# Optimization experiments

Hardware: AMD Instinct MI355X
Metric: run time of the kernel (lower is better)

## Reference

```python
import jax, jax.numpy as jnp
import numpy as np
import math

ITERATIONS = 2
STRIDE = 1
ALPHA = 0.0
MEAN_DATA = 1.0
FINAL_LAMBDA = 0.01  # final_beta
EPS = 1e-7
MIN_VAR_ADD = 0.0005


def setup_inputs() -> dict:
    key = jax.random.key(0)
    k1, k2 = jax.random.split(key)
    b, h, w, k, i, o, a = 2, 12, 12, 3, 32, 32, 4
    votes = jax.random.normal(k1, (b, h, w, k, k, i, o, a, a), dtype=jnp.float32)
    acts = jax.random.uniform(k2, (b, h, w, k, k, i, 1, 1, 1), dtype=jnp.float32)
    beta_a = jnp.full((1, 1, 1, 1, 1, 1, o, 1, 1), 0.5, dtype=jnp.float32)
    beta_u = jnp.full((1, 1, 1, 1, 1, 1, o, 1, 1), 0.5, dtype=jnp.float32)
    return {"votes": votes, "acts": acts, "beta_a": beta_a, "beta_u": beta_u}


def reference(votes, acts, beta_a, beta_u):
    b, h, w, k = votes.shape[0], votes.shape[1], votes.shape[2], votes.shape[3]
    i, o, a = votes.shape[5], votes.shape[6], votes.shape[7]
    s = STRIDE
    Hr = h * s + k - s  # reconstructed height
    Wr = w * s + k - s
    # target spatial coords for each (h,y) / (w,x) of the kernel window
    Y = jnp.arange(h)[:, None] * s + jnp.arange(k)[None, :]  # (h,k)
    X = jnp.arange(w)[:, None] * s + jnp.arange(k)[None, :]  # (w,k)
    lin = (Y[:, None, :, None] * Wr + X[None, :, None, :]).reshape(-1)  # (h*w*k*k,)

    # R_ij init: softmax over zeros along out-capsule axis -> uniform 1/o
    R = jnp.full((b, h, w, k, k, i, o, 1, 1), 1.0 / o, dtype=votes.dtype)
    out_poses = jnp.zeros((b, h, w, 1, 1, 1, o, a, a), dtype=votes.dtype)

    def m_step(R, out_poses, it):
        Ra = R * acts                                   # (b,h,w,k,k,i,o,1,1)
        sumR = jnp.sum(Ra, axis=(3, 4, 5), keepdims=True)
        mu = jnp.sum(Ra * votes, axis=(3, 4, 5), keepdims=True) / (sumR + EPS)
        mu = (1.0 - ALPHA) * mu + ALPHA * out_poses     # (b,h,w,1,1,1,o,a,a)
        sig = jnp.sum(Ra * jnp.square(votes - mu), axis=(3, 4, 5), keepdims=True) / (sumR + EPS) + MIN_VAR_ADD
        cost = (beta_u - 0.5 * jnp.log(sig + EPS)) * sumR / MEAN_DATA
        inv_temp = FINAL_LAMBDA * (1.0 - 0.95 ** (it + 1))
        a_j = jax.nn.sigmoid(inv_temp * (beta_a - jnp.sum(cost, axis=(-1, -2), keepdims=True)))
        return mu, sig, a_j

    def e_step(mu, sig, a_j):
        log_p = -jnp.sum(jnp.log(2.0 * math.pi * sig) + jnp.square(votes - mu) / (2.0 * sig),
                         axis=(-1, -2), keepdims=True)        # (b,h,w,k,k,i,o,1,1)
        lognum = jnp.log(a_j) + log_p
        ap = jnp.exp(lognum - jnp.max(lognum))                # global-max shift as in original
        # scatter-add (fold / col2im) onto the reconstructed grid, then sum over o
        ap6 = ap.reshape(b, h, w, k, k, i, o)
        ap_t = ap6.transpose(1, 2, 3, 4, 0, 5, 6).reshape(h * w * k * k, b, i, o)
        dense = jax.ops.segment_sum(ap_t, lin, num_segments=Hr * Wr)  # (Hr*Wr,b,i,o)
        dense = dense.sum(-1).reshape(Hr, Wr, b, i)
        # extract_patches: gather the window sums back to (b,h,w,k,k,i)
        denom = dense[Y[:, None, :, None], X[None, :, None, :]]  # (h,w,k,k,b,i)
        denom = jnp.transpose(denom, (4, 0, 1, 2, 3, 5))[..., None, None, None]
        return ap / (denom + EPS)

    for it in range(ITERATIONS - 1):
        mu, sig, a_j = m_step(R, out_poses, it)
        out_poses = mu
        R = e_step(mu, sig, a_j)
    mu, sig, a_j = m_step(R, out_poses, ITERATIONS)

    poses = jnp.squeeze(mu, axis=(3, 4, 5))     # (b,h,w,o,a,a)
    acts_out = jnp.squeeze(a_j, axis=(3, 4, 5))  # (b,h,w,o,1,1)
    return poses, acts_out
```

## Files before the change

### kernel.cpp

```cpp
#include <hip/hip_runtime.h>
#include <math.h>

#define NB 2
#define NH 12
#define NW 12
#define NK 3
#define NI 32
#define NO 32
#define NBHW (NB*NH*NW)
#define NC (NK*NK*NI)
#define VPB (NC*NO*16)
#define HR 14
#define WR 14
#define EPSF 1e-7f
#define MINVAR 5e-4f
#define TEMP0 0.0005f
#define TEMPF 0.00142625f

#define CH 4
#define CPC (NC/CH)
#define NBLK (NBHW*CH)
#define ITERS (CPC/2)

#define DENSE_N (NB*HR*WR*NI)
#define DENSE_OFF 0
#define S1_OFF    (DENSE_OFF + DENSE_N)
#define S2_OFF    (S1_OFF + NBLK*512)
#define SR_OFF    (S2_OFF + NBLK*512)
#define MU_OFF    (SR_OFF + NBLK)
#define W_OFF     (MU_OFF + NBHW*512)
#define L_OFF     (W_OFF + NBHW*512)
#define BM_OFF    (L_OFF + NBHW*32)
#define M_OFF     (BM_OFF + NBLK)
#define LOG_OFF   (M_OFF + 4)
#define DSR_OFF   (LOG_OFF + NBHW*NC*NO)

__global__ __launch_bounds__(256) void kA(const float* __restrict__ votes,
        const float* __restrict__ acts, float* __restrict__ ws) {
    __shared__ float s_acts[CPC];
    __shared__ float4 r1[128], r2[128];
    __shared__ float sR1;
    const int bid = blockIdx.x;
    const int bhw = bid >> 2;
    const int cbase = (bid & 3) * CPC;
    const int t = threadIdx.x;
    {
        const int idx = bid*256 + t;
        if (idx < DENSE_N) ws[DENSE_OFF + idx] = 0.f;
    }
    if (t < CPC) s_acts[t] = acts[bhw*NC + cbase + t] * (1.0f/NO);
    __syncthreads();
    const int child_sub = t >> 7;
    const int rem = t & 127;
    const float4* vb4 = (const float4*)votes + (size_t)bhw*(VPB/4);
    float s1[4] = {0,0,0,0}, s2[4] = {0,0,0,0};
    float sumR = 0.f;
    #pragma unroll 6
    for (int it = 0; it < ITERS; ++it) {
        const int c_loc = it*2 + child_sub;
        float4 v = vb4[(size_t)(cbase + c_loc)*128 + rem];
        float ra = s_acts[c_loc];
        s1[0] += ra*v.x; s2[0] = fmaf(ra*v.x, v.x, s2[0]);
        s1[1] += ra*v.y; s2[1] = fmaf(ra*v.y, v.y, s2[1]);
        s1[2] += ra*v.z; s2[2] = fmaf(ra*v.z, v.z, s2[2]);
        s1[3] += ra*v.w; s2[3] = fmaf(ra*v.w, v.w, s2[3]);
        sumR += ra;
    }
    if (child_sub) {
        r1[rem] = make_float4(s1[0], s1[1], s1[2], s1[3]);
        r2[rem] = make_float4(s2[0], s2[1], s2[2], s2[3]);
        if (rem == 0) sR1 = sumR;
    }
    __syncthreads();
    if (!child_sub) {
        float4 o1 = r1[rem], o2 = r2[rem];
        ((float4*)(ws + S1_OFF))[bid*128 + rem] =
            make_float4(s1[0]+o1.x, s1[1]+o1.y, s1[2]+o1.z, s1[3]+o1.w);
        ((float4*)(ws + S2_OFF))[bid*128 + rem] =
            make_float4(s2[0]+o2.x, s2[1]+o2.y, s2[2]+o2.z, s2[3]+o2.w);
        if (rem == 0) ws[SR_OFF + bid] = sumR + sR1;
    }
}

__global__ __launch_bounds__(256) void kB0(const float* __restrict__ beta_a,
        const float* __restrict__ beta_u, float* __restrict__ ws) {
    const int bhw = blockIdx.x;
    const int t = threadIdx.x;
    float sumR = 0.f;
    #pragma unroll
    for (int s = 0; s < CH; ++s) sumR += ws[SR_OFF + bhw*CH + s];
    #pragma unroll
    for (int half = 0; half < 2; ++half) {
        const int idx = t + half*256;
        float s1 = 0.f, s2 = 0.f;
        #pragma unroll
        for (int s = 0; s < CH; ++s) {
            s1 += ws[S1_OFF + (size_t)(bhw*CH + s)*512 + idx];
            s2 += ws[S2_OFF + (size_t)(bhw*CH + s)*512 + idx];
        }
        const int o = idx >> 4, a = idx & 15;
        float mu  = s1 / (sumR + EPSF);
        float sig = (s2 - mu*(2.f*s1 - mu*sumR)) / (sumR + EPSF) + MINVAR;
        ws[MU_OFF + bhw*512 + a*32 + o] = mu;
        ws[W_OFF  + bhw*512 + a*32 + o] = 0.5f / sig;
        float cost = (beta_u[o] - 0.5f*logf(sig + EPSF)) * sumR;
        float ps   = logf(6.2831853071795864f * sig);
        #pragma unroll
        for (int d = 1; d < 16; d <<= 1) {
            cost += __shfl_xor(cost, d);
            ps   += __shfl_xor(ps, d);
        }
        if (a == 0) {
            float aj = 1.0f/(1.0f + expf(-TEMP0*(beta_a[o] - cost)));
            ws[L_OFF + bhw*32 + o] = logf(aj) - ps;
        }
    }
}

__global__ __launch_bounds__(256) void kB(const float* __restrict__ votes,
        float* __restrict__ ws) {
    __shared__ float s_mu[512], s_w[512], s_L[32], smax[4];
    const int bid = blockIdx.x;
    const int bhw = bid >> 2;
    const int cbase = (bid & 3) * CPC;
    const int t = threadIdx.x;
    s_mu[t]     = ws[MU_OFF + bhw*512 + t];
    s_mu[t+256] = ws[MU_OFF + bhw*512 + t + 256];
    s_w[t]      = ws[W_OFF + bhw*512 + t];
    s_w[t+256]  = ws[W_OFF + bhw*512 + t + 256];
    if (t < 32) s_L[t] = ws[L_OFF + bhw*32 + t];
    __syncthreads();
    const int child_sub = t >> 7;
    const int rem = t & 127;
    const int o = rem >> 2;
    const int quad = rem & 3;
    float mur[4], wr[4];
    #pragma unroll
    for (int j = 0; j < 4; ++j) {
        mur[j] = s_mu[(quad*4 + j)*32 + o];
        wr[j]  = s_w [(quad*4 + j)*32 + o];
    }
    const float L = s_L[o];
    const float4* vb4 = (const float4*)votes + (size_t)bhw*(VPB/4);
    float* lp = ws + LOG_OFF + (size_t)bhw*(NC*NO);
    float tmax = -3.0e38f;
    #pragma unroll 6
    for (int it = 0; it < ITERS; ++it) {
        const int c = cbase + it*2 + child_sub;
        float4 v = vb4[(size_t)c*128 + rem];
        float d0 = v.x - mur[0];
        float acc = d0*d0*wr[0];
        float d1 = v.y - mur[1]; acc = fmaf(d1*d1, wr[1], acc);
        float d2 = v.z - mur[2]; acc = fmaf(d2*d2, wr[2], acc);
        float d3 = v.w - mur[3]; acc = fmaf(d3*d3, wr[3], acc);
        acc += __shfl_xor(acc, 1);
        acc += __shfl_xor(acc, 2);
        float ln = L - acc;
        if (quad == 0) lp[c*32 + o] = ln;
        tmax = fmaxf(tmax, ln);
    }
    #pragma unroll
    for (int d = 1; d < 64; d <<= 1) tmax = fmaxf(tmax, __shfl_xor(tmax, d));
    if ((t & 63) == 0) smax[t >> 6] = tmax;
    __syncthreads();
    if (t == 0)
        ws[BM_OFF + bid] = fmaxf(fmaxf(smax[0], smax[1]), fmaxf(smax[2], smax[3]));
}

__global__ __launch_bounds__(256) void kC0(float* __restrict__ ws) {
    __shared__ float smax[4];
    const int t = threadIdx.x;
    float m = -3.0e38f;
    for (int i = t; i < NBLK; i += 256) m = fmaxf(m, ws[BM_OFF + i]);
    #pragma unroll
    for (int d = 1; d < 64; d <<= 1) m = fmaxf(m, __shfl_xor(m, d));
    if ((t & 63) == 0) smax[t >> 6] = m;
    __syncthreads();
    if (t == 0)
        ws[M_OFF] = fmaxf(fmaxf(smax[0], smax[1]), fmaxf(smax[2], smax[3]));
}

__global__ __launch_bounds__(256) void kC(float* __restrict__ ws) {
    const int bid = blockIdx.x;
    const int bhw = bid >> 2;
    const int cbase = (bid & 3) * CPC;
    const int t = threadIdx.x;
    const float M = ws[M_OFF];
    const int b = bhw / (NH*NW);
    const int rem = bhw % (NH*NW);
    const int y = rem / NW, x = rem % NW;
    const float* lp = ws + LOG_OFF + (size_t)bhw*(NC*NO);
    float* dense = ws + DENSE_OFF;
    const int o = t & 31;
    for (int it = 0; it < CPC/8; ++it) {
        const int c = cbase + it*8 + (t >> 5);
        float s = expf(lp[c*32 + o] - M);
        #pragma unroll
        for (int d = 1; d < 32; d <<= 1) s += __shfl_xor(s, d);
        if (o == 0) {
            const int i = c & 31, kk = c >> 5;
            const int ky = kk / 3, kx = kk % 3;
            atomicAdd(&dense[((b*HR + y+ky)*WR + (x+kx))*NI + i], s);
        }
    }
}

__global__ __launch_bounds__(256) void kD(const float* __restrict__ votes,
        const float* __restrict__ acts, float* __restrict__ ws) {
    __shared__ float s_rd[CPC];
    __shared__ float s_ra[CPC*NO];
    __shared__ float4 r1[128], r2[128];
    __shared__ float sSR[64];
    const int bid = blockIdx.x;
    const int bhw = bid >> 2;
    const int cbase = (bid & 3) * CPC;
    const int t = threadIdx.x;
    const int b = bhw / (NH*NW);
    const int remhw = bhw % (NH*NW);
    const int y = remhw / NW, x = remhw % NW;
    const float M = ws[M_OFF];
    if (t < CPC) {
        const int c = cbase + t;
        const int i = c & 31, kk = c >> 5;
        const int ky = kk / 3, kx = kk % 3;
        float dn = ws[DENSE_OFF + ((b*HR + y+ky)*WR + (x+kx))*NI + i];
        s_rd[t] = acts[bhw*NC + c] / (dn + EPSF);
    }
    __syncthreads();
    const float* lp = ws + LOG_OFF + (size_t)bhw*(NC*NO) + (size_t)cbase*32;
    for (int idx = t; idx < CPC*NO; idx += 256)
        s_ra[idx] = s_rd[idx >> 5] * expf(lp[idx] - M);
    __syncthreads();
    const int child_sub = t >> 7;
    const int rem = t & 127;
    const int o = rem >> 2;
    const int quad = rem & 3;
    const float4* vb4 = (const float4*)votes + (size_t)bhw*(VPB/4);
    float s1[4] = {0,0,0,0}, s2[4] = {0,0,0,0};
    float sumR = 0.f;
    #pragma unroll 6
    for (int it = 0; it < ITERS; ++it) {
        const int c_loc = it*2 + child_sub;
        float4 v = vb4[(size_t)(cbase + c_loc)*128 + rem];
        float ra = s_ra[c_loc*32 + o];
        s1[0] += ra*v.x; s2[0] = fmaf(ra*v.x, v.x, s2[0]);
        s1[1] += ra*v.y; s2[1] = fmaf(ra*v.y, v.y, s2[1]);
        s1[2] += ra*v.z; s2[2] = fmaf(ra*v.z, v.z, s2[2]);
        s1[3] += ra*v.w; s2[3] = fmaf(ra*v.w, v.w, s2[3]);
        sumR += ra;
    }
    if (quad == 0) sSR[child_sub*32 + o] = sumR;
    if (child_sub) {
        r1[rem] = make_float4(s1[0], s1[1], s1[2], s1[3]);
        r2[rem] = make_float4(s2[0], s2[1], s2[2], s2[3]);
    }
    __syncthreads();
    if (!child_sub) {
        float4 o1 = r1[rem], o2 = r2[rem];
        ((float4*)(ws + S1_OFF))[bid*128 + rem] =
            make_float4(s1[0]+o1.x, s1[1]+o1.y, s1[2]+o1.z, s1[3]+o1.w);
        ((float4*)(ws + S2_OFF))[bid*128 + rem] =
            make_float4(s2[0]+o2.x, s2[1]+o2.y, s2[2]+o2.z, s2[3]+o2.w);
    }
    if (t < 32) ws[DSR_OFF + bid*32 + t] = sSR[t] + sSR[32 + t];
}

__global__ __launch_bounds__(256) void kD2(const float* __restrict__ beta_a,
        const float* __restrict__ beta_u, const float* __restrict__ ws,
        float* __restrict__ out) {
    const int bid = blockIdx.x;
    const int bhw = bid >> 1;
    const int obase = (bid & 1) * 16;
    const int t = threadIdx.x;
    const int a = t & 15;
    const int o = obase + (t >> 4);
    float s1 = 0.f, s2 = 0.f, sumR = 0.f;
    #pragma unroll
    for (int ch = 0; ch < CH; ++ch) {
        s1   += ws[S1_OFF + (size_t)(bhw*CH + ch)*512 + obase*16 + t];
        s2   += ws[S2_OFF + (size_t)(bhw*CH + ch)*512 + obase*16 + t];
        sumR += ws[DSR_OFF + (bhw*CH + ch)*32 + o];
    }
    float mu  = s1 / (sumR + EPSF);
    float sig = (s2 - mu*(2.f*s1 - mu*sumR)) / (sumR + EPSF) + MINVAR;
    out[bhw*512 + obase*16 + t] = mu;
    float cost = (beta_u[o] - 0.5f*logf(sig + EPSF)) * sumR;
    #pragma unroll
    for (int d = 1; d < 16; d <<= 1) cost += __shfl_xor(cost, d);
    if (a == 0) {
        float aj = 1.0f/(1.0f + expf(-TEMPF*(beta_a[o] - cost)));
        out[NBHW*512 + bhw*32 + o] = aj;
    }
}

extern "C" void kernel_launch(void* const* d_in, const int* in_sizes, int n_in,
                              void* d_out, int out_size, void* d_ws, size_t ws_size,
                              hipStream_t stream) {
    const float* votes  = (const float*)d_in[0];
    const float* acts   = (const float*)d_in[1];
    const float* beta_a = (const float*)d_in[2];
    const float* beta_u = (const float*)d_in[3];
    float* ws  = (float*)d_ws;
    float* out = (float*)d_out;

    kA <<<NBLK,   256, 0, stream>>>(votes, acts, ws);
    kB0<<<NBHW,   256, 0, stream>>>(beta_a, beta_u, ws);
    kB <<<NBLK,   256, 0, stream>>>(votes, ws);
    kC0<<<1,      256, 0, stream>>>(ws);
    kC <<<NBLK,   256, 0, stream>>>(ws);
    kD <<<NBLK,   256, 0, stream>>>(votes, acts, ws);
    kD2<<<NBHW*2, 256, 0, stream>>>(beta_a, beta_u, ws, out);
}
```

Before: 311.1 us.

## Fold reduction kernels into producers via last-block atomic counters

Removes kB0, kC0 and kD2 as separate launches. The per-position finalization now runs in the last arriving block of kA and kD, which is detected with an agent-scope atomic counter and release/acquire fences. The global max is recomputed redundantly in every kC block instead of in a single-block kernel. This cuts launch count and inter-kernel gaps, at the cost of a memset for the counters, redundant max reductions, and serialized tail work in the last block.

Measured after the change: 400.8 us. +28.8%, slower.

```diff
diff --git a/kernel.cpp b/kernel.cpp
--- a/kernel.cpp
+++ b/kernel.cpp
@@ -22,8 +22,9 @@
 #define NBLK (NBHW*CH)
 #define ITERS (CPC/2)
 
+#define CNT_N 576
 #define DENSE_N (NB*HR*WR*NI)
-#define DENSE_OFF 0
+#define DENSE_OFF CNT_N
 #define S1_OFF    (DENSE_OFF + DENSE_N)
 #define S2_OFF    (S1_OFF + NBLK*512)
 #define SR_OFF    (S2_OFF + NBLK*512)
@@ -36,10 +37,12 @@
 #define DSR_OFF   (LOG_OFF + NBHW*NC*NO)
 
 __global__ __launch_bounds__(256) void kA(const float* __restrict__ votes,
-        const float* __restrict__ acts, float* __restrict__ ws) {
+        const float* __restrict__ acts, const float* __restrict__ beta_a,
+        const float* __restrict__ beta_u, float* __restrict__ ws) {
     __shared__ float s_acts[CPC];
     __shared__ float4 r1[128], r2[128];
     __shared__ float sR1;
+    __shared__ int lastf;
     const int bid = blockIdx.x;
     const int bhw = bid >> 2;
     const int cbase = (bid & 3) * CPC;
@@ -80,39 +83,43 @@
             make_float4(s2[0]+o2.x, s2[1]+o2.y, s2[2]+o2.z, s2[3]+o2.w);
         if (rem == 0) ws[SR_OFF + bid] = sumR + sR1;
     }
-}
-
-__global__ __launch_bounds__(256) void kB0(const float* __restrict__ beta_a,
-        const float* __restrict__ beta_u, float* __restrict__ ws) {
-    const int bhw = blockIdx.x;
-    const int t = threadIdx.x;
-    float sumR = 0.f;
-    #pragma unroll
-    for (int s = 0; s < CH; ++s) sumR += ws[SR_OFF + bhw*CH + s];
-    #pragma unroll
-    for (int half = 0; half < 2; ++half) {
-        const int idx = t + half*256;
-        float s1 = 0.f, s2 = 0.f;
+    __syncthreads();
+    if (t == 0) {
+        unsigned prev = __hip_atomic_fetch_add((unsigned*)ws + bhw, 1u,
+                            __ATOMIC_RELEASE, __HIP_MEMORY_SCOPE_AGENT);
+        lastf = (prev == CH - 1);
+        if (lastf) __builtin_amdgcn_fence(__ATOMIC_ACQUIRE, "agent");
+    }
+    __syncthreads();
+    if (lastf) {
+        float sR = 0.f;
         #pragma unroll
-        for (int s = 0; s < CH; ++s) {
-            s1 += ws[S1_OFF + (size_t)(bhw*CH + s)*512 + idx];
-            s2 += ws[S2_OFF + (size_t)(bhw*CH + s)*512 + idx];
-        }
-        const int o = idx >> 4, a = idx & 15;
-        float mu  = s1 / (sumR + EPSF);
-        float sig = (s2 - mu*(2.f*s1 - mu*sumR)) / (sumR + EPSF) + MINVAR;
-        ws[MU_OFF + bhw*512 + a*32 + o] = mu;
-        ws[W_OFF  + bhw*512 + a*32 + o] = 0.5f / sig;
-        float cost = (beta_u[o] - 0.5f*logf(sig + EPSF)) * sumR;
-        float ps   = logf(6.2831853071795864f * sig);
+        for (int s = 0; s < CH; ++s) sR += ws[SR_OFF + bhw*CH + s];
         #pragma unroll
-        for (int d = 1; d < 16; d <<= 1) {
-            cost += __shfl_xor(cost, d);
-            ps   += __shfl_xor(ps, d);
-        }
-        if (a == 0) {
-            float aj = 1.0f/(1.0f + expf(-TEMP0*(beta_a[o] - cost)));
-            ws[L_OFF + bhw*32 + o] = logf(aj) - ps;
+        for (int half = 0; half < 2; ++half) {
+            const int idx = t + half*256;
+            float a1 = 0.f, a2 = 0.f;
+            #pragma unroll
+            for (int s = 0; s < CH; ++s) {
+                a1 += ws[S1_OFF + (size_t)(bhw*CH + s)*512 + idx];
+                a2 += ws[S2_OFF + (size_t)(bhw*CH + s)*512 + idx];
+            }
+            const int o = idx >> 4, a = idx & 15;
+            float mu  = a1 / (sR + EPSF);
+            float sig = (a2 - mu*(2.f*a1 - mu*sR)) / (sR + EPSF) + MINVAR;
+            ws[MU_OFF + bhw*512 + a*32 + o] = mu;
+            ws[W_OFF  + bhw*512 + a*32 + o] = 0.5f / sig;
+            float cost = (beta_u[o] - 0.5f*logf(sig + EPSF)) * sR;
+            float ps   = logf(6.2831853071795864f * sig);
+            #pragma unroll
+            for (int d = 1; d < 16; d <<= 1) {
+                cost += __shfl_xor(cost, d);
+                ps   += __shfl_xor(ps, d);
+            }
+            if (a == 0) {
+                float aj = 1.0f/(1.0f + expf(-TEMP0*(beta_a[o] - cost)));
+                ws[L_OFF + bhw*32 + o] = logf(aj) - ps;
+            }
         }
     }
 }
@@ -167,8 +174,11 @@
         ws[BM_OFF + bid] = fmaxf(fmaxf(smax[0], smax[1]), fmaxf(smax[2], smax[3]));
 }
 
-__global__ __launch_bounds__(256) void kC0(float* __restrict__ ws) {
+__global__ __launch_bounds__(256) void kC(float* __restrict__ ws) {
     __shared__ float smax[4];
+    const int bid = blockIdx.x;
+    const int bhw = bid >> 2;
+    const int cbase = (bid & 3) * CPC;
     const int t = threadIdx.x;
     float m = -3.0e38f;
     for (int i = t; i < NBLK; i += 256) m = fmaxf(m, ws[BM_OFF + i]);
@@ -176,16 +186,8 @@
     for (int d = 1; d < 64; d <<= 1) m = fmaxf(m, __shfl_xor(m, d));
     if ((t & 63) == 0) smax[t >> 6] = m;
     __syncthreads();
-    if (t == 0)
-        ws[M_OFF] = fmaxf(fmaxf(smax[0], smax[1]), fmaxf(smax[2], smax[3]));
-}
-
-__global__ __launch_bounds__(256) void kC(float* __restrict__ ws) {
-    const int bid = blockIdx.x;
-    const int bhw = bid >> 2;
-    const int cbase = (bid & 3) * CPC;
-    const int t = threadIdx.x;
-    const float M = ws[M_OFF];
+    const float M = fmaxf(fmaxf(smax[0], smax[1]), fmaxf(smax[2], smax[3]));
+    if (bid == 0 && t == 0) ws[M_OFF] = M;
     const int b = bhw / (NH*NW);
     const int rem = bhw % (NH*NW);
     const int y = rem / NW, x = rem % NW;
@@ -206,11 +208,14 @@
 }
 
 __global__ __launch_bounds__(256) void kD(const float* __restrict__ votes,
-        const float* __restrict__ acts, float* __restrict__ ws) {
+        const float* __restrict__ acts, const float* __restrict__ beta_a,
+        const float* __restrict__ beta_u, float* __restrict__ ws,
+        float* __restrict__ out) {
     __shared__ float s_rd[CPC];
     __shared__ float s_ra[CPC*NO];
     __shared__ float4 r1[128], r2[128];
     __shared__ float sSR[64];
+    __shared__ int lastf;
     const int bid = blockIdx.x;
     const int bhw = bid >> 2;
     const int cbase = (bid & 3) * CPC;
@@ -263,33 +268,37 @@
             make_float4(s2[0]+o2.x, s2[1]+o2.y, s2[2]+o2.z, s2[3]+o2.w);
     }
     if (t < 32) ws[DSR_OFF + bid*32 + t] = sSR[t] + sSR[32 + t];
-}
-
-__global__ __launch_bounds__(256) void kD2(const float* __restrict__ beta_a,
-        const float* __restrict__ beta_u, const float* __restrict__ ws,
-        float* __restrict__ out) {
-    const int bid = blockIdx.x;
-    const int bhw = bid >> 1;
-    const int obase = (bid & 1) * 16;
-    const int t = threadIdx.x;
-    const int a = t & 15;
-    const int o = obase + (t >> 4);
-    float s1 = 0.f, s2 = 0.f, sumR = 0.f;
-    #pragma unroll
-    for (int ch = 0; ch < CH; ++ch) {
-        s1   += ws[S1_OFF + (size_t)(bhw*CH + ch)*512 + obase*16 + t];
-        s2   += ws[S2_OFF + (size_t)(bhw*CH + ch)*512 + obase*16 + t];
-        sumR += ws[DSR_OFF + (bhw*CH + ch)*32 + o];
-    }
-    float mu  = s1 / (sumR + EPSF);
-    float sig = (s2 - mu*(2.f*s1 - mu*sumR)) / (sumR + EPSF) + MINVAR;
-    out[bhw*512 + obase*16 + t] = mu;
-    float cost = (beta_u[o] - 0.5f*logf(sig + EPSF)) * sumR;
-    #pragma unroll
-    for (int d = 1; d < 16; d <<= 1) cost += __shfl_xor(cost, d);
-    if (a == 0) {
-        float aj = 1.0f/(1.0f + expf(-TEMPF*(beta_a[o] - cost)));
-        out[NBHW*512 + bhw*32 + o] = aj;
+    __syncthreads();
+    if (t == 0) {
+        unsigned prev = __hip_atomic_fetch_add((unsigned*)ws + NBHW + bhw, 1u,
+                            __ATOMIC_RELEASE, __HIP_MEMORY_SCOPE_AGENT);
+        lastf = (prev == CH - 1);
+        if (lastf) __builtin_amdgcn_fence(__ATOMIC_ACQUIRE, "agent");
+    }
+    __syncthreads();
+    if (lastf) {
+        #pragma unroll
+        for (int half = 0; half < 2; ++half) {
+            const int idx = t + half*256;
+            const int oo = idx >> 4, a = idx & 15;
+            float a1 = 0.f, a2 = 0.f, sR = 0.f;
+            #pragma unroll
+            for (int ch = 0; ch < CH; ++ch) {
+                a1 += ws[S1_OFF + (size_t)(bhw*CH + ch)*512 + idx];
+                a2 += ws[S2_OFF + (size_t)(bhw*CH + ch)*512 + idx];
+                sR += ws[DSR_OFF + (bhw*CH + ch)*32 + oo];
+            }
+            float mu  = a1 / (sR + EPSF);
+            float sig = (a2 - mu*(2.f*a1 - mu*sR)) / (sR + EPSF) + MINVAR;
+            out[bhw*512 + idx] = mu;
+            float cost = (beta_u[oo] - 0.5f*logf(sig + EPSF)) * sR;
+            #pragma unroll
+            for (int d = 1; d < 16; d <<= 1) cost += __shfl_xor(cost, d);
+            if (a == 0) {
+                float aj = 1.0f/(1.0f + expf(-TEMPF*(beta_a[oo] - cost)));
+                out[NBHW*512 + bhw*32 + oo] = aj;
+            }
+        }
     }
 }
 
@@ -303,11 +312,9 @@
     float* ws  = (float*)d_ws;
     float* out = (float*)d_out;
 
-    kA <<<NBLK,   256, 0, stream>>>(votes, acts, ws);
-    kB0<<<NBHW,   256, 0, stream>>>(beta_a, beta_u, ws);
-    kB <<<NBLK,   256, 0, stream>>>(votes, ws);
-    kC0<<<1,      256, 0, stream>>>(ws);
-    kC <<<NBLK,   256, 0, stream>>>(ws);
-    kD <<<NBLK,   256, 0, stream>>>(votes, acts, ws);
-    kD2<<<NBHW*2, 256, 0, stream>>>(beta_a, beta_u, ws, out);
-}
+    hipMemsetAsync(d_ws, 0, CNT_N*sizeof(float), stream);
+    kA<<<NBLK, 256, 0, stream>>>(votes, acts, beta_a, beta_u, ws);
+    kB<<<NBLK, 256, 0, stream>>>(votes, ws);
+    kC<<<NBLK, 256, 0, stream>>>(ws);
+    kD<<<NBLK, 256, 0, stream>>>(votes, acts, beta_a, beta_u, ws, out);
+}
```

## Fuse EM routing into three kernels partitioned by output-capsule pairs

Applied to the files above, without the earlier changes.

Replaces the seven-kernel pipeline with three. Each block now handles one spatial position and two output capsules, and stages that slice of votes in LDS so the first M-step, E-step log-probabilities and block max run in a single kernel without re-reading votes from global memory. The global-max kernel is folded into the col2im kernel, and the final M-step is fused with its reduction and output. This removes launch overhead and intermediate workspace round-trips, but each block now reads strided 32-byte chunks of votes and uses about 37KB of LDS, which may lower occupancy and coalescing.

After: 285.9 us. 1.09x faster.

```diff
diff --git a/kernel.cpp b/kernel.cpp
--- a/kernel.cpp
+++ b/kernel.cpp
@@ -17,147 +17,105 @@
 #define TEMP0 0.0005f
 #define TEMPF 0.00142625f
 
-#define CH 4
-#define CPC (NC/CH)
-#define NBLK (NBHW*CH)
-#define ITERS (CPC/2)
+#define OGRP 16
+#define GF (NBHW*OGRP)
+#define LDSROW 289
 
 #define DENSE_N (NB*HR*WR*NI)
 #define DENSE_OFF 0
-#define S1_OFF    (DENSE_OFF + DENSE_N)
-#define S2_OFF    (S1_OFF + NBLK*512)
-#define SR_OFF    (S2_OFF + NBLK*512)
-#define MU_OFF    (SR_OFF + NBLK)
-#define W_OFF     (MU_OFF + NBHW*512)
-#define L_OFF     (W_OFF + NBHW*512)
-#define BM_OFF    (L_OFF + NBHW*32)
-#define M_OFF     (BM_OFF + NBLK)
-#define LOG_OFF   (M_OFF + 4)
-#define DSR_OFF   (LOG_OFF + NBHW*NC*NO)
-
-__global__ __launch_bounds__(256) void kA(const float* __restrict__ votes,
-        const float* __restrict__ acts, float* __restrict__ ws) {
-    __shared__ float s_acts[CPC];
-    __shared__ float4 r1[128], r2[128];
-    __shared__ float sR1;
+#define BM_OFF  (DENSE_OFF + DENSE_N)
+#define M_OFF   (BM_OFF + GF)
+#define LP_OFF  (M_OFF + 4)
+
+__global__ __launch_bounds__(256) void kF1(const float* __restrict__ votes,
+        const float* __restrict__ acts, const float* __restrict__ beta_a,
+        const float* __restrict__ beta_u, float* __restrict__ ws) {
+    __shared__ float lds_v[32][LDSROW];
+    __shared__ float s_acts[NC];
+    __shared__ float red[3][8][32];
+    __shared__ float s_mu[32], s_w[32], s_L[2], smax[4];
     const int bid = blockIdx.x;
-    const int bhw = bid >> 2;
-    const int cbase = (bid & 3) * CPC;
+    const int bhw = bid >> 4;
+    const int o0 = (bid & 15) * 2;
     const int t = threadIdx.x;
-    {
-        const int idx = bid*256 + t;
+    #pragma unroll
+    for (int j = 0; j < 3; ++j) {
+        const int idx = bid*3 + j;
         if (idx < DENSE_N) ws[DENSE_OFF + idx] = 0.f;
     }
-    if (t < CPC) s_acts[t] = acts[bhw*NC + cbase + t] * (1.0f/NO);
-    __syncthreads();
-    const int child_sub = t >> 7;
-    const int rem = t & 127;
-    const float4* vb4 = (const float4*)votes + (size_t)bhw*(VPB/4);
-    float s1[4] = {0,0,0,0}, s2[4] = {0,0,0,0};
-    float sumR = 0.f;
-    #pragma unroll 6
-    for (int it = 0; it < ITERS; ++it) {
-        const int c_loc = it*2 + child_sub;
-        float4 v = vb4[(size_t)(cbase + c_loc)*128 + rem];
-        float ra = s_acts[c_loc];
-        s1[0] += ra*v.x; s2[0] = fmaf(ra*v.x, v.x, s2[0]);
-        s1[1] += ra*v.y; s2[1] = fmaf(ra*v.y, v.y, s2[1]);
-        s1[2] += ra*v.z; s2[2] = fmaf(ra*v.z, v.z, s2[2]);
-        s1[3] += ra*v.w; s2[3] = fmaf(ra*v.w, v.w, s2[3]);
-        sumR += ra;
-    }
-    if (child_sub) {
-        r1[rem] = make_float4(s1[0], s1[1], s1[2], s1[3]);
-        r2[rem] = make_float4(s2[0], s2[1], s2[2], s2[3]);
-        if (rem == 0) sR1 = sumR;
-    }
-    __syncthreads();
-    if (!child_sub) {
-        float4 o1 = r1[rem], o2 = r2[rem];
-        ((float4*)(ws + S1_OFF))[bid*128 + rem] =
-            make_float4(s1[0]+o1.x, s1[1]+o1.y, s1[2]+o1.z, s1[3]+o1.w);
-        ((float4*)(ws + S2_OFF))[bid*128 + rem] =
-            make_float4(s2[0]+o2.x, s2[1]+o2.y, s2[2]+o2.z, s2[3]+o2.w);
-        if (rem == 0) ws[SR_OFF + bid] = sumR + sR1;
-    }
-}
-
-__global__ __launch_bounds__(256) void kB0(const float* __restrict__ beta_a,
-        const float* __restrict__ beta_u, float* __restrict__ ws) {
-    const int bhw = blockIdx.x;
-    const int t = threadIdx.x;
-    float sumR = 0.f;
-    #pragma unroll
-    for (int s = 0; s < CH; ++s) sumR += ws[SR_OFF + bhw*CH + s];
-    #pragma unroll
-    for (int half = 0; half < 2; ++half) {
-        const int idx = t + half*256;
-        float s1 = 0.f, s2 = 0.f;
-        #pragma unroll
-        for (int s = 0; s < CH; ++s) {
-            s1 += ws[S1_OFF + (size_t)(bhw*CH + s)*512 + idx];
-            s2 += ws[S2_OFF + (size_t)(bhw*CH + s)*512 + idx];
-        }
-        const int o = idx >> 4, a = idx & 15;
-        float mu  = s1 / (sumR + EPSF);
-        float sig = (s2 - mu*(2.f*s1 - mu*sumR)) / (sumR + EPSF) + MINVAR;
-        ws[MU_OFF + bhw*512 + a*32 + o] = mu;
-        ws[W_OFF  + bhw*512 + a*32 + o] = 0.5f / sig;
-        float cost = (beta_u[o] - 0.5f*logf(sig + EPSF)) * sumR;
+    s_acts[t] = acts[bhw*NC + t] * (1.0f/NO);
+    if (t < 32) s_acts[256 + t] = acts[bhw*NC + 256 + t] * (1.0f/NO);
+    const float4* vb4 = (const float4*)votes + (size_t)bhw*(VPB/4) + o0*4;
+    {
+        const int f = t & 7;
+        const int cof = t >> 3;
+        #pragma unroll
+        for (int cb = 0; cb < 9; ++cb) {
+            const int c = cb*32 + cof;
+            float4 v = vb4[(size_t)c*128 + f];
+            lds_v[f*4+0][c] = v.x;
+            lds_v[f*4+1][c] = v.y;
+            lds_v[f*4+2][c] = v.z;
+            lds_v[f*4+3][c] = v.w;
+        }
+    }
+    __syncthreads();
+    {
+        const int c_sub = t >> 5, e = t & 31;
+        float s1 = 0.f, s2 = 0.f, sR = 0.f;
+        #pragma unroll 6
+        for (int k = 0; k < 36; ++k) {
+            const int c = k*8 + c_sub;
+            float v = lds_v[e][c];
+            float ra = s_acts[c];
+            s1 += ra*v; s2 = fmaf(ra*v, v, s2); sR += ra;
+        }
+        red[0][c_sub][e] = s1; red[1][c_sub][e] = s2; red[2][c_sub][e] = sR;
+    }
+    __syncthreads();
+    if (t < 32) {
+        const int e = t;
+        float s1 = 0.f, s2 = 0.f, sR = 0.f;
+        #pragma unroll
+        for (int cs = 0; cs < 8; ++cs) {
+            s1 += red[0][cs][e]; s2 += red[1][cs][e]; sR += red[2][cs][e];
+        }
+        const int o = o0 + (e >> 4);
+        float mu  = s1 / (sR + EPSF);
+        float sig = (s2 - mu*(2.f*s1 - mu*sR)) / (sR + EPSF) + MINVAR;
+        s_mu[e] = mu;
+        s_w[e]  = 0.5f / sig;
+        float cost = (beta_u[o] - 0.5f*logf(sig + EPSF)) * sR;
         float ps   = logf(6.2831853071795864f * sig);
         #pragma unroll
         for (int d = 1; d < 16; d <<= 1) {
             cost += __shfl_xor(cost, d);
             ps   += __shfl_xor(ps, d);
         }
-        if (a == 0) {
+        if ((e & 15) == 0) {
             float aj = 1.0f/(1.0f + expf(-TEMP0*(beta_a[o] - cost)));
-            ws[L_OFF + bhw*32 + o] = logf(aj) - ps;
-        }
-    }
-}
-
-__global__ __launch_bounds__(256) void kB(const float* __restrict__ votes,
-        float* __restrict__ ws) {
-    __shared__ float s_mu[512], s_w[512], s_L[32], smax[4];
-    const int bid = blockIdx.x;
-    const int bhw = bid >> 2;
-    const int cbase = (bid & 3) * CPC;
-    const int t = threadIdx.x;
-    s_mu[t]     = ws[MU_OFF + bhw*512 + t];
-    s_mu[t+256] = ws[MU_OFF + bhw*512 + t + 256];
-    s_w[t]      = ws[W_OFF + bhw*512 + t];
-    s_w[t+256]  = ws[W_OFF + bhw*512 + t + 256];
-    if (t < 32) s_L[t] = ws[L_OFF + bhw*32 + t];
-    __syncthreads();
-    const int child_sub = t >> 7;
-    const int rem = t & 127;
-    const int o = rem >> 2;
-    const int quad = rem & 3;
-    float mur[4], wr[4];
-    #pragma unroll
-    for (int j = 0; j < 4; ++j) {
-        mur[j] = s_mu[(quad*4 + j)*32 + o];
-        wr[j]  = s_w [(quad*4 + j)*32 + o];
-    }
-    const float L = s_L[o];
-    const float4* vb4 = (const float4*)votes + (size_t)bhw*(VPB/4);
-    float* lp = ws + LOG_OFF + (size_t)bhw*(NC*NO);
+            s_L[e >> 4] = logf(aj) - ps;
+        }
+    }
+    __syncthreads();
+    float* lpt = ws + LP_OFF + (size_t)bhw*(NC*NO) + (size_t)o0*NC;
     float tmax = -3.0e38f;
-    #pragma unroll 6
-    for (int it = 0; it < ITERS; ++it) {
-        const int c = cbase + it*2 + child_sub;
-        float4 v = vb4[(size_t)c*128 + rem];
-        float d0 = v.x - mur[0];
-        float acc = d0*d0*wr[0];
-        float d1 = v.y - mur[1]; acc = fmaf(d1*d1, wr[1], acc);
-        float d2 = v.z - mur[2]; acc = fmaf(d2*d2, wr[2], acc);
-        float d3 = v.w - mur[3]; acc = fmaf(d3*d3, wr[3], acc);
-        acc += __shfl_xor(acc, 1);
-        acc += __shfl_xor(acc, 2);
-        float ln = L - acc;
-        if (quad == 0) lp[c*32 + o] = ln;
-        tmax = fmaxf(tmax, ln);
+    #pragma unroll
+    for (int pass = 0; pass < 2; ++pass) {
+        const int c = pass*256 + t;
+        if (c < NC) {
+            float acc0 = 0.f, acc1 = 0.f;
+            #pragma unroll
+            for (int e = 0; e < 16; ++e) {
+                float d0 = lds_v[e][c]    - s_mu[e];
+                acc0 = fmaf(d0*d0, s_w[e], acc0);
+                float d1 = lds_v[e+16][c] - s_mu[e+16];
+                acc1 = fmaf(d1*d1, s_w[e+16], acc1);
+            }
+            float ln0 = s_L[0] - acc0, ln1 = s_L[1] - acc1;
+            lpt[c] = ln0; lpt[NC + c] = ln1;
+            tmax = fmaxf(tmax, fmaxf(ln0, ln1));
+        }
     }
     #pragma unroll
     for (int d = 1; d < 64; d <<= 1) tmax = fmaxf(tmax, __shfl_xor(tmax, d));
@@ -167,37 +125,29 @@
         ws[BM_OFF + bid] = fmaxf(fmaxf(smax[0], smax[1]), fmaxf(smax[2], smax[3]));
 }
 
-__global__ __launch_bounds__(256) void kC0(float* __restrict__ ws) {
+__global__ __launch_bounds__(256) void kC(float* __restrict__ ws) {
     __shared__ float smax[4];
+    const int bhw = blockIdx.x;
     const int t = threadIdx.x;
     float m = -3.0e38f;
-    for (int i = t; i < NBLK; i += 256) m = fmaxf(m, ws[BM_OFF + i]);
+    for (int i = t; i < GF; i += 256) m = fmaxf(m, ws[BM_OFF + i]);
     #pragma unroll
     for (int d = 1; d < 64; d <<= 1) m = fmaxf(m, __shfl_xor(m, d));
     if ((t & 63) == 0) smax[t >> 6] = m;
     __syncthreads();
-    if (t == 0)
-        ws[M_OFF] = fmaxf(fmaxf(smax[0], smax[1]), fmaxf(smax[2], smax[3]));
-}
-
-__global__ __launch_bounds__(256) void kC(float* __restrict__ ws) {
-    const int bid = blockIdx.x;
-    const int bhw = bid >> 2;
-    const int cbase = (bid & 3) * CPC;
-    const int t = threadIdx.x;
-    const float M = ws[M_OFF];
+    const float M = fmaxf(fmaxf(smax[0], smax[1]), fmaxf(smax[2], smax[3]));
+    if (bhw == 0 && t == 0) ws[M_OFF] = M;
     const int b = bhw / (NH*NW);
     const int rem = bhw % (NH*NW);
     const int y = rem / NW, x = rem % NW;
-    const float* lp = ws + LOG_OFF + (size_t)bhw*(NC*NO);
+    const float* lpt = ws + LP_OFF + (size_t)bhw*(NC*NO);
     float* dense = ws + DENSE_OFF;
-    const int o = t & 31;
-    for (int it = 0; it < CPC/8; ++it) {
-        const int c = cbase + it*8 + (t >> 5);
-        float s = expf(lp[c*32 + o] - M);
-        #pragma unroll
-        for (int d = 1; d < 32; d <<= 1) s += __shfl_xor(s, d);
-        if (o == 0) {
+    #pragma unroll
+    for (int pass = 0; pass < 2; ++pass) {
+        const int c = pass*256 + t;
+        if (c < NC) {
+            float s = 0.f;
+            for (int o = 0; o < NO; ++o) s += expf(lpt[(size_t)o*NC + c] - M);
             const int i = c & 31, kk = c >> 5;
             const int ky = kk / 3, kx = kk % 3;
             atomicAdd(&dense[((b*HR + y+ky)*WR + (x+kx))*NI + i], s);
@@ -205,91 +155,81 @@
     }
 }
 
-__global__ __launch_bounds__(256) void kD(const float* __restrict__ votes,
-        const float* __restrict__ acts, float* __restrict__ ws) {
-    __shared__ float s_rd[CPC];
-    __shared__ float s_ra[CPC*NO];
-    __shared__ float4 r1[128], r2[128];
-    __shared__ float sSR[64];
+__global__ __launch_bounds__(256) void kF3(const float* __restrict__ votes,
+        const float* __restrict__ acts, const float* __restrict__ beta_a,
+        const float* __restrict__ beta_u, float* __restrict__ ws,
+        float* __restrict__ out) {
+    __shared__ float lds_v[32][LDSROW];
+    __shared__ float s_ra[2][NC];
+    __shared__ float red[3][8][32];
     const int bid = blockIdx.x;
-    const int bhw = bid >> 2;
-    const int cbase = (bid & 3) * CPC;
+    const int bhw = bid >> 4;
+    const int o0 = (bid & 15) * 2;
     const int t = threadIdx.x;
     const int b = bhw / (NH*NW);
     const int remhw = bhw % (NH*NW);
     const int y = remhw / NW, x = remhw % NW;
     const float M = ws[M_OFF];
-    if (t < CPC) {
-        const int c = cbase + t;
-        const int i = c & 31, kk = c >> 5;
-        const int ky = kk / 3, kx = kk % 3;
-        float dn = ws[DENSE_OFF + ((b*HR + y+ky)*WR + (x+kx))*NI + i];
-        s_rd[t] = acts[bhw*NC + c] / (dn + EPSF);
-    }
-    __syncthreads();
-    const float* lp = ws + LOG_OFF + (size_t)bhw*(NC*NO) + (size_t)cbase*32;
-    for (int idx = t; idx < CPC*NO; idx += 256)
-        s_ra[idx] = s_rd[idx >> 5] * expf(lp[idx] - M);
-    __syncthreads();
-    const int child_sub = t >> 7;
-    const int rem = t & 127;
-    const int o = rem >> 2;
-    const int quad = rem & 3;
-    const float4* vb4 = (const float4*)votes + (size_t)bhw*(VPB/4);
-    float s1[4] = {0,0,0,0}, s2[4] = {0,0,0,0};
-    float sumR = 0.f;
-    #pragma unroll 6
-    for (int it = 0; it < ITERS; ++it) {
-        const int c_loc = it*2 + child_sub;
-        float4 v = vb4[(size_t)(cbase + c_loc)*128 + rem];
-        float ra = s_ra[c_loc*32 + o];
-        s1[0] += ra*v.x; s2[0] = fmaf(ra*v.x, v.x, s2[0]);
-        s1[1] += ra*v.y; s2[1] = fmaf(ra*v.y, v.y, s2[1]);
-        s1[2] += ra*v.z; s2[2] = fmaf(ra*v.z, v.z, s2[2]);
-        s1[3] += ra*v.w; s2[3] = fmaf(ra*v.w, v.w, s2[3]);
-        sumR += ra;
-    }
-    if (quad == 0) sSR[child_sub*32 + o] = sumR;
-    if (child_sub) {
-        r1[rem] = make_float4(s1[0], s1[1], s1[2], s1[3]);
-        r2[rem] = make_float4(s2[0], s2[1], s2[2], s2[3]);
-    }
-    __syncthreads();
-    if (!child_sub) {
-        float4 o1 = r1[rem], o2 = r2[rem];
-        ((float4*)(ws + S1_OFF))[bid*128 + rem] =
-            make_float4(s1[0]+o1.x, s1[1]+o1.y, s1[2]+o1.z, s1[3]+o1.w);
-        ((float4*)(ws + S2_OFF))[bid*128 + rem] =
-            make_float4(s2[0]+o2.x, s2[1]+o2.y, s2[2]+o2.z, s2[3]+o2.w);
-    }
-    if (t < 32) ws[DSR_OFF + bid*32 + t] = sSR[t] + sSR[32 + t];
-}
-
-__global__ __launch_bounds__(256) void kD2(const float* __restrict__ beta_a,
-        const float* __restrict__ beta_u, const float* __restrict__ ws,
-        float* __restrict__ out) {
-    const int bid = blockIdx.x;
-    const int bhw = bid >> 1;
-    const int obase = (bid & 1) * 16;
-    const int t = threadIdx.x;
-    const int a = t & 15;
-    const int o = obase + (t >> 4);
-    float s1 = 0.f, s2 = 0.f, sumR = 0.f;
-    #pragma unroll
-    for (int ch = 0; ch < CH; ++ch) {
-        s1   += ws[S1_OFF + (size_t)(bhw*CH + ch)*512 + obase*16 + t];
-        s2   += ws[S2_OFF + (size_t)(bhw*CH + ch)*512 + obase*16 + t];
-        sumR += ws[DSR_OFF + (bhw*CH + ch)*32 + o];
-    }
-    float mu  = s1 / (sumR + EPSF);
-    float sig = (s2 - mu*(2.f*s1 - mu*sumR)) / (sumR + EPSF) + MINVAR;
-    out[bhw*512 + obase*16 + t] = mu;
-    float cost = (beta_u[o] - 0.5f*logf(sig + EPSF)) * sumR;
-    #pragma unroll
-    for (int d = 1; d < 16; d <<= 1) cost += __shfl_xor(cost, d);
-    if (a == 0) {
-        float aj = 1.0f/(1.0f + expf(-TEMPF*(beta_a[o] - cost)));
-        out[NBHW*512 + bhw*32 + o] = aj;
+    const float* lpt = ws + LP_OFF + (size_t)bhw*(NC*NO) + (size_t)o0*NC;
+    #pragma unroll
+    for (int pass = 0; pass < 2; ++pass) {
+        const int c = pass*256 + t;
+        if (c < NC) {
+            const int i = c & 31, kk = c >> 5;
+            const int ky = kk / 3, kx = kk % 3;
+            float dn = ws[DENSE_OFF + ((b*HR + y+ky)*WR + (x+kx))*NI + i];
+            float r = acts[bhw*NC + c] / (dn + EPSF);
+            s_ra[0][c] = r * expf(lpt[c] - M);
+            s_ra[1][c] = r * expf(lpt[NC + c] - M);
+        }
+    }
+    const float4* vb4 = (const float4*)votes + (size_t)bhw*(VPB/4) + o0*4;
+    {
+        const int f = t & 7;
+        const int cof = t >> 3;
+        #pragma unroll
+        for (int cb = 0; cb < 9; ++cb) {
+            const int c = cb*32 + cof;
+            float4 v = vb4[(size_t)c*128 + f];
+            lds_v[f*4+0][c] = v.x;
+            lds_v[f*4+1][c] = v.y;
+            lds_v[f*4+2][c] = v.z;
+            lds_v[f*4+3][c] = v.w;
+        }
+    }
+    __syncthreads();
+    {
+        const int c_sub = t >> 5, e = t & 31;
+        const int o_sub = e >> 4;
+        float s1 = 0.f, s2 = 0.f, sR = 0.f;
+        #pragma unroll 6
+        for (int k = 0; k < 36; ++k) {
+            const int c = k*8 + c_sub;
+            float v = lds_v[e][c];
+            float ra = s_ra[o_sub][c];
+            s1 += ra*v; s2 = fmaf(ra*v, v, s2); sR += ra;
+        }
+        red[0][c_sub][e] = s1; red[1][c_sub][e] = s2; red[2][c_sub][e] = sR;
+    }
+    __syncthreads();
+    if (t < 32) {
+        const int e = t;
+        float s1 = 0.f, s2 = 0.f, sR = 0.f;
+        #pragma unroll
+        for (int cs = 0; cs < 8; ++cs) {
+            s1 += red[0][cs][e]; s2 += red[1][cs][e]; sR += red[2][cs][e];
+        }
+        const int o = o0 + (e >> 4);
+        float mu  = s1 / (sR + EPSF);
+        float sig = (s2 - mu*(2.f*s1 - mu*sR)) / (sR + EPSF) + MINVAR;
+        out[bhw*512 + o0*16 + e] = mu;
+        float cost = (beta_u[o] - 0.5f*logf(sig + EPSF)) * sR;
+        #pragma unroll
+        for (int d = 1; d < 16; d <<= 1) cost += __shfl_xor(cost, d);
+        if ((e & 15) == 0) {
+            float aj = 1.0f/(1.0f + expf(-TEMPF*(beta_a[o] - cost)));
+            out[NBHW*512 + bhw*32 + o] = aj;
+        }
     }
 }
 
@@ -303,11 +243,7 @@
     float* ws  = (float*)d_ws;
     float* out = (float*)d_out;
 
-    kA <<<NBLK,   256, 0, stream>>>(votes, acts, ws);
-    kB0<<<NBHW,   256, 0, stream>>>(beta_a, beta_u, ws);
-    kB <<<NBLK,   256, 0, stream>>>(votes, ws);
-    kC0<<<1,      256, 0, stream>>>(ws);
-    kC <<<NBLK,   256, 0, stream>>>(ws);
-    kD <<<NBLK,   256, 0, stream>>>(votes, acts, ws);
-    kD2<<<NBHW*2, 256, 0, stream>>>(beta_a, beta_u, ws, out);
-}
+    kF1<<<GF,   256, 0, stream>>>(votes, acts, beta_a, beta_u, ws);
+    kC <<<NBHW, 256, 0, stream>>>(ws);
+    kF3<<<GF,   256, 0, stream>>>(votes, acts, beta_a, beta_u, ws, out);
+}
```
